# Kernel optimization log

Hardware: AMD Instinct MI355X
Metric: run time of the kernel (lower is better)

The kernel has to match this reference:

```python
import jax, jax.numpy as jnp
import numpy as np

N, D = 2048, 32


def setup_inputs() -> dict:
    key = jax.random.key(0)
    k1, k2, k3, k4 = jax.random.split(key, 4)
    x = jax.random.normal(k1, (N, D), dtype=jnp.float32)
    # positive hyperparameters (Gamma-prior samples in the original)
    lengthscale = jax.random.uniform(k2, (D,), dtype=jnp.float32, minval=0.5, maxval=2.0)
    alpha = jax.random.uniform(k3, (), dtype=jnp.float32, minval=0.5, maxval=2.0)
    outputscale = jax.random.uniform(k4, (), dtype=jnp.float32, minval=0.5, maxval=2.0)
    return {"x": x, "lengthscale": lengthscale, "alpha": alpha, "outputscale": outputscale}


def reference(x, lengthscale, alpha, outputscale):
    # Additive RQ kernel: k(xi, xj) = outputscale * sum_d (1 + ((xi_d - xj_d)/l_d)^2 / (2*alpha))^(-alpha)
    xs = x / lengthscale                      # [N, D]
    d2 = (xs[:, None, :] - xs[None, :, :]) ** 2   # [N, N, D] per-dim squared distance
    covar = outputscale * jnp.sum((1.0 + d2 / (2.0 * alpha)) ** (-alpha), axis=-1)  # [N, N]
    mean = jnp.zeros((x.shape[0],), dtype=x.dtype)  # ZeroMean
    return mean, covar
```

## Files before the change

kernel.cpp:

```cpp
#include <hip/hip_runtime.h>


#define D 32
#define TILE 32

#if __has_builtin(__builtin_amdgcn_exp2f)
#define EXP2F(x) __builtin_amdgcn_exp2f(x)
#else
#define EXP2F(x) exp2f(x)
#endif
#if __has_builtin(__builtin_amdgcn_logf)
#define LOG2F(x) __builtin_amdgcn_logf(x)
#else
#define LOG2F(x) __log2f(x)
#endif

__global__ __launch_bounds__(256) void rq_covar_sym_kernel(
    const float* __restrict__ x,
    const float* __restrict__ ls,
    const float* __restrict__ alpha_p,
    const float* __restrict__ os_p,
    float* __restrict__ mean_out,
    float* __restrict__ covar,
    int n, int ntiles)
{
    __shared__ float As[TILE][36];
    __shared__ float Bs[TILE][36];

    const int t = threadIdx.x;
    const int k = blockIdx.x;

    {
        const int idx = k * 256 + t;
        if (idx < n) mean_out[idx] = 0.0f;
    }

    const float nt = (float)ntiles;
    int bi = (int)(nt + 0.5f - sqrtf((nt + 0.5f) * (nt + 0.5f) - 2.0f * (float)k));
    while (bi > 0 && k < bi * ntiles - (bi * (bi - 1)) / 2) --bi;
    while (k >= (bi + 1) * ntiles - ((bi + 1) * bi) / 2) ++bi;
    const int bj = bi + (k - (bi * ntiles - (bi * (bi - 1)) / 2));

    const float alpha = alpha_p[0];
    const float oscale = os_p[0];
    const float nalpha = -alpha;
    const float rs2a = rsqrtf(2.0f * alpha);

    {
        const int row = t >> 3;
        const int q = (t & 7) * 4;
        const float4 lv = *reinterpret_cast<const float4*>(&ls[q]);
        const float4 a = *reinterpret_cast<const float4*>(&x[(size_t)(bi * TILE + row) * D + q]);
        const float4 b = *reinterpret_cast<const float4*>(&x[(size_t)(bj * TILE + row) * D + q]);
        const float w0 = rs2a / lv.x, w1 = rs2a / lv.y, w2 = rs2a / lv.z, w3 = rs2a / lv.w;
        As[row][q + 0] = a.x * w0;  Bs[row][q + 0] = b.x * w0;
        As[row][q + 1] = a.y * w1;  Bs[row][q + 1] = b.y * w1;
        As[row][q + 2] = a.z * w2;  Bs[row][q + 2] = b.z * w2;
        As[row][q + 3] = a.w * w3;  Bs[row][q + 3] = b.w * w3;
    }
    __syncthreads();

    const int c = t & 31;
    const int r0 = t >> 5;

    float bs[D];
#pragma unroll
    for (int q = 0; q < D; q += 4) {
        const float4 v = *reinterpret_cast<const float4*>(&Bs[c][q]);
        bs[q] = v.x; bs[q + 1] = v.y; bs[q + 2] = v.z; bs[q + 3] = v.w;
    }

    float acc[4];
#pragma unroll
    for (int kk = 0; kk < 4; ++kk) {
        const int r = r0 + kk * 8;
        float as[D];
#pragma unroll
        for (int q = 0; q < D; q += 4) {
            const float4 v = *reinterpret_cast<const float4*>(&As[r][q]);
            as[q] = v.x; as[q + 1] = v.y; as[q + 2] = v.z; as[q + 3] = v.w;
        }
        float s0 = 0.0f, s1 = 0.0f;
#pragma unroll
        for (int d = 0; d < D; d += 2) {
            const float diff0 = as[d] - bs[d];
            const float base0 = fmaf(diff0, diff0, 1.0f);
            s0 += EXP2F(nalpha * LOG2F(base0));
            const float diff1 = as[d + 1] - bs[d + 1];
            const float base1 = fmaf(diff1, diff1, 1.0f);
            s1 += EXP2F(nalpha * LOG2F(base1));
        }
        acc[kk] = oscale * (s0 + s1);
    }

#pragma unroll
    for (int kk = 0; kk < 4; ++kk) {
        const int r = r0 + kk * 8;
        covar[(size_t)(bi * TILE + r) * n + (bj * TILE + c)] = acc[kk];
    }

    if (bi != bj) {
        __syncthreads();
#pragma unroll
        for (int kk = 0; kk < 4; ++kk) {
            As[r0 + kk * 8][c] = acc[kk];
        }
        __syncthreads();
#pragma unroll
        for (int kk = 0; kk < 4; ++kk) {
            const int rr = r0 + kk * 8;
            const float v = As[c][rr];
            covar[(size_t)(bj * TILE + rr) * n + (bi * TILE + c)] = v;
        }
    }
}

extern "C" void kernel_launch(void* const* d_in, const int* in_sizes, int n_in,
                              void* d_out, int out_size, void* d_ws, size_t ws_size,
                              hipStream_t stream) {
    const float* x = (const float*)d_in[0];
    const float* ls = (const float*)d_in[1];
    const float* alpha_p = (const float*)d_in[2];
    const float* os_p = (const float*)d_in[3];

    const int n = in_sizes[0] / D;
    const int ntiles = n / TILE;
    const int nblocks = ntiles * (ntiles + 1) / 2;

    float* mean_out = (float*)d_out;
    float* covar = (float*)d_out + n;

    rq_covar_sym_kernel<<<nblocks, 256, 0, stream>>>(x, ls, alpha_p, os_p,
                                                     mean_out, covar, n, ntiles);
}
```

Measured before the change: 81.36 us.

## Replace per-element log2/exp2 power with exponent table and mantissa polynomial

```diff
diff --git a/kernel.cpp b/kernel.cpp
--- a/kernel.cpp
+++ b/kernel.cpp
@@ -26,6 +26,7 @@
 {
     __shared__ float As[TILE][36];
     __shared__ float Bs[TILE][36];
+    __shared__ float pow2tab[160];
 
     const int t = threadIdx.x;
     const int k = blockIdx.x;
@@ -45,6 +46,34 @@
     const float oscale = os_p[0];
     const float nalpha = -alpha;
     const float rs2a = rsqrtf(2.0f * alpha);
+
+    for (int e = t; e < 160; e += 256)
+        pow2tab[e] = EXP2F(nalpha * (float)(e - 127));
+
+    const float Xc[8] = {1.990393f, 1.915735f, 1.777785f, 1.597545f,
+                         1.402455f, 1.222215f, 1.084265f, 1.009607f};
+    float dd[8];
+#pragma unroll
+    for (int i = 0; i < 8; ++i)
+        dd[i] = EXP2F(nalpha * LOG2F(Xc[i]));
+#pragma unroll
+    for (int j = 1; j < 8; ++j) {
+#pragma unroll
+        for (int i = 7; i >= 1; --i) {
+            if (i >= j)
+                dd[i] = (dd[i] - dd[i - 1]) * (1.0f / (Xc[i] - Xc[i - j]));
+        }
+    }
+    float C[8] = {0.0f, 0.0f, 0.0f, 0.0f, 0.0f, 0.0f, 0.0f, 0.0f};
+    C[0] = dd[7];
+#pragma unroll
+    for (int i = 6; i >= 0; --i) {
+        const float yi = Xc[i] - 1.5f;
+#pragma unroll
+        for (int kk = 7; kk >= 1; --kk)
+            C[kk] = fmaf(-yi, C[kk], C[kk - 1]);
+        C[0] = fmaf(-yi, C[0], dd[i]);
+    }
 
     {
         const int row = t >> 3;
@@ -80,17 +109,32 @@
             const float4 v = *reinterpret_cast<const float4*>(&As[r][q]);
             as[q] = v.x; as[q + 1] = v.y; as[q + 2] = v.z; as[q + 3] = v.w;
         }
-        float s0 = 0.0f, s1 = 0.0f;
+        float s0 = 0.0f, s1 = 0.0f, s2 = 0.0f, s3 = 0.0f;
 #pragma unroll
-        for (int d = 0; d < D; d += 2) {
-            const float diff0 = as[d] - bs[d];
-            const float base0 = fmaf(diff0, diff0, 1.0f);
-            s0 += EXP2F(nalpha * LOG2F(base0));
-            const float diff1 = as[d + 1] - bs[d + 1];
-            const float base1 = fmaf(diff1, diff1, 1.0f);
-            s1 += EXP2F(nalpha * LOG2F(base1));
+        for (int d = 0; d < D; d += 4) {
+#pragma unroll
+            for (int j = 0; j < 4; ++j) {
+                const float diff = as[d + j] - bs[d + j];
+                const float tv = fmaf(diff, diff, 1.0f);
+                const unsigned bits = __float_as_uint(tv);
+                const float pw = pow2tab[bits >> 23];
+                const float m = __uint_as_float((bits & 0x7FFFFFu) | 0x3F800000u);
+                const float sm = m - 1.5f;
+                float p = fmaf(C[7], sm, C[6]);
+                p = fmaf(p, sm, C[5]);
+                p = fmaf(p, sm, C[4]);
+                p = fmaf(p, sm, C[3]);
+                p = fmaf(p, sm, C[2]);
+                p = fmaf(p, sm, C[1]);
+                p = fmaf(p, sm, C[0]);
+                const float term_pw = pw;
+                if (j == 0) s0 = fmaf(p, term_pw, s0);
+                else if (j == 1) s1 = fmaf(p, term_pw, s1);
+                else if (j == 2) s2 = fmaf(p, term_pw, s2);
+                else s3 = fmaf(p, term_pw, s3);
+            }
         }
-        acc[kk] = oscale * (s0 + s1);
+        acc[kk] = oscale * ((s0 + s1) + (s2 + s3));
     }
 
 #pragma unroll
```

After: 85.71 us. +5.4%, slower.
